# Kernel optimization log

Hardware: AMD Instinct MI355X
Metric: run time of the kernel (lower is better)

Reference implementation:

```python
import jax, jax.numpy as jnp
import numpy as np

B, N, E = 16, 2048, 1024
G, V = 2, 320
D = E // G
TAU = 2.0


def setup_inputs() -> dict:
    key = jax.random.key(0)
    k1, k2, k3, k4 = jax.random.split(key, 4)
    x = jax.random.normal(k1, (B, N, E), dtype=jnp.float32)
    u = jax.random.uniform(k2, (B, N, G, V), dtype=jnp.float32)
    W = jax.random.normal(k3, (E, G * V), dtype=jnp.float32) * 0.02
    b = jnp.zeros((G * V,), dtype=jnp.float32)
    codebook = jax.random.normal(k4, (G, V, D), dtype=jnp.float32)
    return {"x": x, "u": u, "W": W, "b": b, "codebook": codebook}


def reference(x, u, W, b, codebook):
    Bx, Nx, Ex = x.shape
    Gx, Vx, Dx = codebook.shape
    # linear projection -> per-group logits [B,N,G,V]
    h = (jnp.einsum('bne,ef->bnf', x, W) + b).reshape(Bx, Nx, Gx, Vx)
    # gumbel noise from uniform samples (clamped away from 0/1)
    eps = 1e-7
    g = -jnp.log(-jnp.log(u * (1.0 - 2.0 * eps) + eps))
    soft = jax.nn.softmax((h + g) / TAU, axis=-1)
    # hard one-hot with straight-through estimator (matches torch hard=True)
    idx = jnp.argmax(soft, axis=-1)
    hard = jax.nn.one_hot(idx, Vx, dtype=soft.dtype)
    y = hard - jax.lax.stop_gradient(soft) + soft  # [B,N,G,V]
    # select code vectors: equivalent to broadcast-mul + sum over V
    code_vector = jnp.einsum('bngv,gvd->bngd', y, codebook).reshape(Bx, Nx, Gx * Dx)
    # codebook usage entropy: sum one-hots over time, softmax over V per group
    p = jax.nn.softmax(jnp.sum(y, axis=1), axis=-1)  # [B,G,V]
    entropy = -jnp.sum(p * jnp.log(p + 1e-8)) / (Gx * Vx)
    return code_vector, entropy
```

## Files before the change

### kernel.cpp

```cpp
#include <hip/hip_runtime.h>

namespace {

constexpr int Bsz = 16, Nsz = 2048, Esz = 1024, Gsz = 2, Vsz = 320, Dsz = 512;
constexpr int Msz = Bsz * Nsz;
constexpr int Fsz = Gsz * Vsz;
constexpr int BM = 128, BN = 128, BK = 32;
constexpr int NKC = Esz / 32;

typedef __attribute__((ext_vector_type(8))) short bf16x8;
typedef __attribute__((ext_vector_type(4))) float f32x4;
typedef unsigned int u32;
typedef unsigned short u16;

__device__ __forceinline__ void load_lds16(const void* g, void* l) {
  __builtin_amdgcn_global_load_lds(
      (const __attribute__((address_space(1))) u32*)g,
      (__attribute__((address_space(3))) u32*)l, 16, 0, 0);
}

__device__ __forceinline__ ushort f2bf(float f) {
  union { float f; unsigned u; } v; v.f = f;
  unsigned r = (v.u + 0x7FFFu + ((v.u >> 16) & 1u)) >> 16;
  return (ushort)r;
}
__device__ __forceinline__ float bf2f(ushort h) {
  union { unsigned u; float f; } v; v.u = ((unsigned)h) << 16;
  return v.f;
}

__device__ __forceinline__ float gumb_precise(float uu) {
  const float C0 = 1.0f - 2.0f * 1e-7f;
  float up = uu * C0;
  up = up + 1e-7f;
  return -logf(-logf(up));
}
__device__ __forceinline__ float gumb_fast(float uu) {
  const float C0 = 1.0f - 2.0f * 1e-7f;
  const float up = fmaf(uu, C0, 1e-7f);
  const float d = 1.0f - up;
  const float ypoly =
      d * fmaf(d, fmaf(d, fmaf(d, fmaf(d, 0.2f, 0.25f), 0.33333334f), 0.5f), 1.0f);
  const float yfast = -__logf(up);
  const float y = (up >= 0.84f) ? ypoly : yfast;
  return -__logf(y);
}

struct Top2 { float v1, v2; int i1, i2; };
__device__ __forceinline__ void t2_feed(Top2& t, float z, int f) {
  if (z > t.v1 || (z == t.v1 && f < t.i1)) {
    t.v2 = t.v1; t.i2 = t.i1; t.v1 = z; t.i1 = f;
  } else if (z > t.v2 || (z == t.v2 && f < t.i2)) {
    t.v2 = z; t.i2 = f;
  }
}
__device__ __forceinline__ void t2_merge(Top2& t, float ov1, int oi1, float ov2,
                                         int oi2) {
  if (ov1 > t.v1 || (ov1 == t.v1 && oi1 < t.i1)) {
    const bool keep = (t.v1 > ov2) || (t.v1 == ov2 && t.i1 < oi2);
    t.v2 = keep ? t.v1 : ov2; t.i2 = keep ? t.i1 : oi2;
    t.v1 = ov1; t.i1 = oi1;
  } else if (ov1 > t.v2 || (ov1 == t.v2 && oi1 < t.i2)) {
    t.v2 = ov1; t.i2 = oi1;
  }
}

__device__ __forceinline__ uint2 pack_hi_trunc(float4 a) {
  uint2 r;
  r.x = (__float_as_uint(a.x) >> 16) | (__float_as_uint(a.y) & 0xffff0000u);
  r.y = (__float_as_uint(a.z) >> 16) | (__float_as_uint(a.w) & 0xffff0000u);
  return r;
}
__device__ __forceinline__ float4 resid_trunc(float4 a) {
  float4 r;
  r.x = a.x - __uint_as_float(__float_as_uint(a.x) & 0xffff0000u);
  r.y = a.y - __uint_as_float(__float_as_uint(a.y) & 0xffff0000u);
  r.z = a.z - __uint_as_float(__float_as_uint(a.z) & 0xffff0000u);
  r.w = a.w - __uint_as_float(__float_as_uint(a.w) & 0xffff0000u);
  return r;
}


__global__ __launch_bounds__(256) void k_prep(const float* __restrict__ W,
                                              u16* __restrict__ wt,
                                              float* __restrict__ wtT) {
  const int tid = threadIdx.x;
  const int l = tid & 63;
  const int blob = blockIdx.x * 4 + (tid >> 6);
  const int fb = blob >> 5, kc = blob & 31;
  const int f = fb * 16 + (l & 15);
  const int k0 = kc * 32 + (l >> 4) * 8;
  float v[8];
  ushort hh[8], ll[8];
#pragma unroll
  for (int j = 0; j < 8; ++j) {
    v[j] = W[(size_t)(k0 + j) * Fsz + f];
    hh[j] = f2bf(v[j]);
    ll[j] = f2bf(v[j] - bf2f(hh[j]));
  }
  uint4 qh, ql;
  qh.x = hh[0] | ((u32)hh[1] << 16); qh.y = hh[2] | ((u32)hh[3] << 16);
  qh.z = hh[4] | ((u32)hh[5] << 16); qh.w = hh[6] | ((u32)hh[7] << 16);
  ql.x = ll[0] | ((u32)ll[1] << 16); ql.y = ll[2] | ((u32)ll[3] << 16);
  ql.z = ll[4] | ((u32)ll[5] << 16); ql.w = ll[6] | ((u32)ll[7] << 16);
  *(uint4*)(wt + ((size_t)blob * 2 + 0) * 512 + l * 8) = qh;
  *(uint4*)(wt + ((size_t)blob * 2 + 1) * 512 + l * 8) = ql;
  float4 t0, t1;
  t0.x = v[0]; t0.y = v[1]; t0.z = v[2]; t0.w = v[3];
  t1.x = v[4]; t1.y = v[5]; t1.z = v[6]; t1.w = v[7];
  *(float4*)(wtT + (size_t)f * Esz + k0) = t0;
  *(float4*)(wtT + (size_t)f * Esz + k0 + 4) = t1;
}

__global__ __launch_bounds__(256) void k_prepx(const float* __restrict__ x,
                                               u16* __restrict__ xt) {
  const int tid = threadIdx.x;
  const int l = tid & 63;
  const int blob = blockIdx.x * 4 + (tid >> 6);
  const int mb = blob >> 5, kc = blob & 31;
  const size_t row = (size_t)mb * 16 + (l & 15);
  const int k0 = kc * 32 + (l >> 4) * 8;
  const float4 a0 = *(const float4*)(x + row * Esz + k0);
  const float4 a1 = *(const float4*)(x + row * Esz + k0 + 4);
  const uint2 h0 = pack_hi_trunc(a0), h1 = pack_hi_trunc(a1);
  const uint2 l0 = pack_hi_trunc(resid_trunc(a0));
  const uint2 l1 = pack_hi_trunc(resid_trunc(a1));
  uint4 qh, ql;
  qh.x = h0.x; qh.y = h0.y; qh.z = h1.x; qh.w = h1.y;
  ql.x = l0.x; ql.y = l0.y; ql.z = l1.x; ql.w = l1.y;
  *(uint4*)(xt + ((size_t)blob * 2 + 0) * 512 + l * 8) = qh;
  *(uint4*)(xt + ((size_t)blob * 2 + 1) * 512 + l * 8) = ql;
}

__global__ __launch_bounds__(256, 3) void k_gemm(
    const float* __restrict__ u, const float* __restrict__ bias,
    const u16* __restrict__ xt, const u16* __restrict__ wt,
    float4* __restrict__ partial) {
  __shared__ __align__(16) u16 sm[24576];

  const int tid = threadIdx.x;
  const int bid = blockIdx.x;
  const int tile = (bid & 7) * 320 + (bid >> 3);
  const int mt = tile / 10, nt = tile - mt * 10;
  const int m0 = mt * BM;
  const int n0 = nt * 64;

  const int lane = tid & 63, w = tid >> 6;
  const int lrow = lane & 15, quad = lane >> 4;

  f32x4 acc[2][4];
#pragma unroll
  for (int i = 0; i < 2; ++i)
#pragma unroll
    for (int j = 0; j < 4; ++j) acc[i][j] = (f32x4){0.f, 0.f, 0.f, 0.f};

  const u16* src0[6];
  int dstoff[6];
#pragma unroll
  for (int i = 0; i < 6; ++i) {
    const int cc = w + 4 * i;
    const int isA = (cc < 16) ? 1 : 0;
    const int c = isA ? cc : (cc - 16);
    const int gb = (isA ? (m0 >> 4) : (n0 >> 4)) + (c >> 1);
    const int p = c & 1;
    src0[i] = (isA ? xt : wt) + ((size_t)gb * NKC * 2 + p) * 512 + lane * 8;
    dstoff[i] = (isA ? 0 : 8192) + c * 512;
  }

  auto stage = [&](int buf, int kc) {
    const size_t go = (size_t)kc * 1024;
#pragma unroll
    for (int i = 0; i < 6; ++i)
      load_lds16(src0[i] + go, sm + buf * 12288 + dstoff[i]);
  };

  stage(0, 0);
  stage(1, 1);
  int cur = 0;

  for (int kc = 0; kc < NKC; ++kc) {
    if (kc < NKC - 1) {
      asm volatile("s_waitcnt vmcnt(6)" ::: "memory");
    } else {
      asm volatile("s_waitcnt vmcnt(0)" ::: "memory");
    }
    __builtin_amdgcn_s_barrier();

    const u16* As = sm + cur * 12288;
    const u16* Bs = As + 8192;
    bf16x8 ah[2], al[2], bh[4], bl[4];
#pragma unroll
    for (int rt = 0; rt < 2; ++rt) {
      const int blk = w * 2 + rt;
      ah[rt] = *(const bf16x8*)(As + (blk * 2 + 0) * 512 + lane * 8);
      al[rt] = *(const bf16x8*)(As + (blk * 2 + 1) * 512 + lane * 8);
    }
#pragma unroll
    for (int ct = 0; ct < 4; ++ct) {
      bh[ct] = *(const bf16x8*)(Bs + (ct * 2 + 0) * 512 + lane * 8);
      bl[ct] = *(const bf16x8*)(Bs + (ct * 2 + 1) * 512 + lane * 8);
    }
    asm volatile("s_waitcnt lgkmcnt(0)" ::: "memory");
    __builtin_amdgcn_sched_barrier(0);
    __builtin_amdgcn_s_barrier();
    if (kc + 2 < NKC) stage(cur, kc + 2);
    __builtin_amdgcn_sched_barrier(0);
#pragma unroll
    for (int ct = 0; ct < 4; ++ct)
#pragma unroll
      for (int rt = 0; rt < 2; ++rt) {
        acc[rt][ct] = __builtin_amdgcn_mfma_f32_16x16x32_bf16(al[rt], bh[ct], acc[rt][ct], 0, 0, 0);
        acc[rt][ct] = __builtin_amdgcn_mfma_f32_16x16x32_bf16(ah[rt], bl[ct], acc[rt][ct], 0, 0, 0);
        acc[rt][ct] = __builtin_amdgcn_mfma_f32_16x16x32_bf16(ah[rt], bh[ct], acc[rt][ct], 0, 0, 0);
      }
    cur ^= 1;
  }

  const int pcol = nt;
#pragma unroll
  for (int rt = 0; rt < 2; ++rt) {
#pragma unroll
    for (int rg = 0; rg < 4; ++rg) {
      const int row = w * 32 + rt * 16 + quad * 4 + rg;
      const size_t m = (size_t)(m0 + row);
      Top2 t; t.v1 = -3.4e38f; t.v2 = -3.4e38f; t.i1 = 1 << 30; t.i2 = 1 << 30;
#pragma unroll
      for (int ct = 0; ct < 4; ++ct) {
        const int f = n0 + ct * 16 + lrow;
        const float z = acc[rt][ct][rg] + bias[f] + gumb_fast(u[m * 640 + f]);
        t2_feed(t, z, f);
      }
#pragma unroll
      for (int off = 1; off < 16; off <<= 1) {
        const float ov1 = __shfl_xor(t.v1, off, 16);
        const int oi1 = __shfl_xor(t.i1, off, 16);
        const float ov2 = __shfl_xor(t.v2, off, 16);
        const int oi2 = __shfl_xor(t.i2, off, 16);
        t2_merge(t, ov1, oi1, ov2, oi2);
      }
      if (lrow == 0) {
        float4 o;
        o.x = t.v1; o.y = __int_as_float(t.i1);
        o.z = t.v2; o.w = __int_as_float(t.i2);
        partial[m * 10 + pcol] = o;
      }
    }
  }
}

__global__ __launch_bounds__(256) void k_select(
    const float4* __restrict__ partial, const float* __restrict__ x,
    const float* __restrict__ wtT, const float* __restrict__ bias,
    const float* __restrict__ u, int2* __restrict__ idx_out,
    int* __restrict__ counts) {
  const int tid = threadIdx.x;
  const size_t m = (size_t)blockIdx.x * 256 + tid;
  int vsel[2];
#pragma unroll
  for (int g = 0; g < 2; ++g) {
    Top2 t; t.v1 = -3.4e38f; t.v2 = -3.4e38f; t.i1 = 1 << 30; t.i2 = 1 << 30;
#pragma unroll
    for (int p = 0; p < 5; ++p) {
      const float4 q = partial[m * 10 + g * 5 + p];
      t2_merge(t, q.x, __float_as_int(q.y), q.z, __float_as_int(q.w));
    }
    int i1 = t.i1;
    if (t.v1 - t.v2 < 1e-3f) {
      const int i2 = t.i2;
      const float* xp = x + m * Esz;
      const float* w1 = wtT + (size_t)i1 * Esz;
      const float* w2 = wtT + (size_t)i2 * Esz;
      float h1 = 0.f, h2 = 0.f;
      for (int k = 0; k < Esz; k += 4) {
        const float4 xv = *(const float4*)(xp + k);
        const float4 a = *(const float4*)(w1 + k);
        const float4 b = *(const float4*)(w2 + k);
        h1 = fmaf(xv.x, a.x, h1); h1 = fmaf(xv.y, a.y, h1);
        h1 = fmaf(xv.z, a.z, h1); h1 = fmaf(xv.w, a.w, h1);
        h2 = fmaf(xv.x, b.x, h2); h2 = fmaf(xv.y, b.y, h2);
        h2 = fmaf(xv.z, b.z, h2); h2 = fmaf(xv.w, b.w, h2);
      }
      const float z1 = h1 + bias[i1] + gumb_precise(u[m * 640 + i1]);
      const float z2 = h2 + bias[i2] + gumb_precise(u[m * 640 + i2]);
      if (z2 > z1 || (z2 == z1 && i2 < i1)) i1 = i2;
    }
    const int v = i1 - g * Vsz;
    vsel[g] = v;
    const int b = (int)(m >> 11);
    atomicAdd(&counts[(b * Gsz + g) * Vsz + v], 1);
  }
  int2 r; r.x = vsel[0]; r.y = vsel[1];
  idx_out[m] = r;
}

__global__ __launch_bounds__(256) void k_gather(const int2* __restrict__ idx,
                                                const float* __restrict__ cb,
                                                float* __restrict__ out) {
  const int tid = threadIdx.x;
  const size_t mbase = (size_t)blockIdx.x * 8;
  const int gq = tid >> 7, dq = tid & 127;
#pragma unroll
  for (int it = 0; it < 8; ++it) {
    const int2 p = idx[mbase + it];
    const int v = gq ? p.y : p.x;
    const float4 cv =
        *(const float4*)(cb + ((size_t)(gq * Vsz + v)) * Dsz + dq * 4);
    *(float4*)(out + (mbase + it) * (size_t)(Gsz * Dsz) + tid * 4) = cv;
  }
}


__global__ __launch_bounds__(256) void k_prep_fb(const float* __restrict__ W,
                                                 u16* __restrict__ wt_h,
                                                 u16* __restrict__ wt_l) {
  const int f = blockIdx.x;
  const int k0 = threadIdx.x * 4;
  float v[4];
#pragma unroll
  for (int i = 0; i < 4; ++i) v[i] = W[(size_t)(k0 + i) * Fsz + f];
  ushort4 hh, ll;
  hh.x = f2bf(v[0]); ll.x = f2bf(v[0] - bf2f(hh.x));
  hh.y = f2bf(v[1]); ll.y = f2bf(v[1] - bf2f(hh.y));
  hh.z = f2bf(v[2]); ll.z = f2bf(v[2] - bf2f(hh.z));
  hh.w = f2bf(v[3]); ll.w = f2bf(v[3] - bf2f(hh.w));
  *(ushort4*)(wt_h + (size_t)f * Esz + k0) = hh;
  *(ushort4*)(wt_l + (size_t)f * Esz + k0) = ll;
}

__global__ __launch_bounds__(256) void k_gemm_fb(
    const float* __restrict__ x, const float* __restrict__ u,
    const float* __restrict__ bias, const u16* __restrict__ wth,
    const u16* __restrict__ wtl, float4* __restrict__ partial) {
  __shared__ __align__(16) u16 sm[16384];
  u16* xs_h = sm;
  u16* xs_l = sm + 4096;
  u16* bs_h = sm + 8192;
  u16* bs_l = sm + 12288;

  const int tid = threadIdx.x;
  const int n0 = blockIdx.x * BN;
  const int m0 = blockIdx.y * BM;
  const int lane = tid & 63, w = tid >> 6;
  const int wr = w >> 1, wc = w & 1;
  const int lrow = lane & 15, quad = lane >> 4;

  f32x4 acc[4][4];
#pragma unroll
  for (int i = 0; i < 4; ++i)
#pragma unroll
    for (int j = 0; j < 4; ++j) acc[i][j] = (f32x4){0.f, 0.f, 0.f, 0.f};

  for (int k0 = 0; k0 < Esz; k0 += BK) {
    float4 av[4];
#pragma unroll
    for (int s = 0; s < 4; ++s) {
      const int id = tid + 256 * s;
      const int row = id >> 3, kq = id & 7;
      av[s] = *(const float4*)(x + (size_t)(m0 + row) * Esz + k0 + kq * 4);
    }
    __syncthreads();
#pragma unroll
    for (int c = 0; c < 4; ++c) {
      const int chunk = w + 4 * c;
      const int plane = chunk >> 3, ch = chunk & 7;
      const u16* src = (plane ? wtl : wth) +
                       (size_t)(n0 + ch * 16 + (lane >> 2)) * Esz + k0 +
                       (lane & 3) * 8;
      u16* dst = (plane ? bs_l : bs_h) + ch * 512;
      load_lds16(src, dst);
    }
#pragma unroll
    for (int s = 0; s < 4; ++s) {
      const int id = tid + 256 * s;
      const int row = id >> 3, kq = id & 7;
      const u32 u0 = __float_as_uint(av[s].x), u1 = __float_as_uint(av[s].y);
      const u32 u2 = __float_as_uint(av[s].z), u3 = __float_as_uint(av[s].w);
      uint2 hh, ll;
      hh.x = (u0 >> 16) | (u1 & 0xffff0000u);
      hh.y = (u2 >> 16) | (u3 & 0xffff0000u);
      const float r0 = av[s].x - __uint_as_float(u0 & 0xffff0000u);
      const float r1 = av[s].y - __uint_as_float(u1 & 0xffff0000u);
      const float r2 = av[s].z - __uint_as_float(u2 & 0xffff0000u);
      const float r3 = av[s].w - __uint_as_float(u3 & 0xffff0000u);
      ll.x = (__float_as_uint(r0) >> 16) | (__float_as_uint(r1) & 0xffff0000u);
      ll.y = (__float_as_uint(r2) >> 16) | (__float_as_uint(r3) & 0xffff0000u);
      *(uint2*)(xs_h + row * 32 + kq * 4) = hh;
      *(uint2*)(xs_l + row * 32 + kq * 4) = ll;
    }
    __syncthreads();

    bf16x8 ah[4], al[4];
#pragma unroll
    for (int rt = 0; rt < 4; ++rt) {
      const int off = (wr * 64 + rt * 16 + lrow) * 32 + quad * 8;
      ah[rt] = *(const bf16x8*)(xs_h + off);
      al[rt] = *(const bf16x8*)(xs_l + off);
    }
#pragma unroll
    for (int ct = 0; ct < 4; ++ct) {
      const int off = (wc * 64 + ct * 16 + lrow) * 32 + quad * 8;
      const bf16x8 bh = *(const bf16x8*)(bs_h + off);
      const bf16x8 bl = *(const bf16x8*)(bs_l + off);
#pragma unroll
      for (int rt = 0; rt < 4; ++rt) {
        acc[rt][ct] = __builtin_amdgcn_mfma_f32_16x16x32_bf16(al[rt], bh, acc[rt][ct], 0, 0, 0);
        acc[rt][ct] = __builtin_amdgcn_mfma_f32_16x16x32_bf16(ah[rt], bl, acc[rt][ct], 0, 0, 0);
        acc[rt][ct] = __builtin_amdgcn_mfma_f32_16x16x32_bf16(ah[rt], bh, acc[rt][ct], 0, 0, 0);
      }
    }
  }

  const int pcol = blockIdx.x * 2 + wc;
#pragma unroll
  for (int rt = 0; rt < 4; ++rt) {
#pragma unroll
    for (int rg = 0; rg < 4; ++rg) {
      const int row = wr * 64 + rt * 16 + quad * 4 + rg;
      const size_t m = (size_t)(m0 + row);
      Top2 t; t.v1 = -3.4e38f; t.v2 = -3.4e38f; t.i1 = 1 << 30; t.i2 = 1 << 30;
#pragma unroll
      for (int ct = 0; ct < 4; ++ct) {
        const int f = n0 + wc * 64 + ct * 16 + lrow;
        const float z = acc[rt][ct][rg] + bias[f] + gumb_fast(u[m * 640 + f]);
        t2_feed(t, z, f);
      }
#pragma unroll
      for (int off = 1; off < 16; off <<= 1) {
        const float ov1 = __shfl_xor(t.v1, off, 16);
        const int oi1 = __shfl_xor(t.i1, off, 16);
        const float ov2 = __shfl_xor(t.v2, off, 16);
        const int oi2 = __shfl_xor(t.i2, off, 16);
        t2_merge(t, ov1, oi1, ov2, oi2);
      }
      if (lrow == 0) {
        float4 o;
        o.x = t.v1; o.y = __int_as_float(t.i1);
        o.z = t.v2; o.w = __int_as_float(t.i2);
        partial[m * 10 + pcol] = o;
      }
    }
  }
}

__global__ __launch_bounds__(256) void k_select_fb(
    const float4* __restrict__ partial, const float* __restrict__ x,
    const float* __restrict__ W, const float* __restrict__ bias,
    const float* __restrict__ u, const float* __restrict__ cb,
    float* __restrict__ out, int* __restrict__ counts) {
  __shared__ int idx_sh[256][2];
  const int tid = threadIdx.x;
  const size_t m = (size_t)blockIdx.x * 256 + tid;

#pragma unroll
  for (int g = 0; g < 2; ++g) {
    Top2 t; t.v1 = -3.4e38f; t.v2 = -3.4e38f; t.i1 = 1 << 30; t.i2 = 1 << 30;
#pragma unroll
    for (int p = 0; p < 5; ++p) {
      const float4 q = partial[m * 10 + g * 5 + p];
      t2_merge(t, q.x, __float_as_int(q.y), q.z, __float_as_int(q.w));
    }
    int i1 = t.i1;
    if (t.v1 - t.v2 < 1e-3f) {
      const int i2 = t.i2;
      const float* xp = x + m * Esz;
      float h1 = 0.f, h2 = 0.f;
      for (int k = 0; k < Esz; ++k) {
        const float xv = xp[k];
        h1 = fmaf(xv, W[(size_t)k * Fsz + i1], h1);
        h2 = fmaf(xv, W[(size_t)k * Fsz + i2], h2);
      }
      const float z1 = h1 + bias[i1] + gumb_precise(u[m * 640 + i1]);
      const float z2 = h2 + bias[i2] + gumb_precise(u[m * 640 + i2]);
      if (z2 > z1 || (z2 == z1 && i2 < i1)) i1 = i2;
    }
    const int v = i1 - g * Vsz;
    idx_sh[tid][g] = v;
    const int b = (int)(m >> 11);
    atomicAdd(&counts[(b * Gsz + g) * Vsz + v], 1);
  }
  __syncthreads();

  const size_t mbase = (size_t)blockIdx.x * 256;
  const int gq = tid >> 7, dq = tid & 127;
  for (int it = 0; it < 256; ++it) {
    const int v = idx_sh[it][gq];
    const float4 cv =
        *(const float4*)(cb + ((size_t)(gq * Vsz + v)) * Dsz + dq * 4);
    *(float4*)(out + (mbase + it) * (size_t)(Gsz * Dsz) + tid * 4) = cv;
  }
}

__global__ __launch_bounds__(64) void k_entropy(const int* __restrict__ counts,
                                                float* __restrict__ partial) {
  const int bg = blockIdx.x;
  const int lane = threadIdx.x;
  float c[5];
  float mx = -3.4e38f;
#pragma unroll
  for (int t = 0; t < 5; ++t) {
    c[t] = (float)counts[bg * Vsz + lane + 64 * t];
    mx = fmaxf(mx, c[t]);
  }
#pragma unroll
  for (int off = 32; off; off >>= 1) mx = fmaxf(mx, __shfl_xor(mx, off));
  float e[5];
  float s = 0.f;
#pragma unroll
  for (int t = 0; t < 5; ++t) {
    e[t] = expf(c[t] - mx);
    s += e[t];
  }
#pragma unroll
  for (int off = 32; off; off >>= 1) s += __shfl_xor(s, off);
  float ent = 0.f;
#pragma unroll
  for (int t = 0; t < 5; ++t) {
    const float p = e[t] / s;
    ent += p * logf(p + 1e-8f);
  }
#pragma unroll
  for (int off = 32; off; off >>= 1) ent += __shfl_xor(ent, off);
  if (lane == 0) partial[bg] = ent;
}

__global__ __launch_bounds__(64) void k_final(const float* __restrict__ partial,
                                              float* __restrict__ dst) {
  const int lane = threadIdx.x;
  float v = (lane < 32) ? partial[lane] : 0.f;
#pragma unroll
  for (int off = 32; off; off >>= 1) v += __shfl_xor(v, off);
  if (lane == 0) dst[0] = -v / (float)(Gsz * Vsz);
}

}

extern "C" void kernel_launch(void* const* d_in, const int* in_sizes, int n_in,
                              void* d_out, int out_size, void* d_ws,
                              size_t ws_size, hipStream_t stream) {
  const float* x = (const float*)d_in[0];
  const float* u = (const float*)d_in[1];
  const float* W = (const float*)d_in[2];
  const float* bias = (const float*)d_in[3];
  const float* cb = (const float*)d_in[4];
  float* out = (float*)d_out;

  int* counts = (int*)d_ws;
  float* epart = (float*)((char*)d_ws + 40960);
  float4* partial = (float4*)((char*)d_ws + 65536);
  const size_t PART_END = 65536 + (size_t)Msz * 10 * 16;
  const size_t NEED_NEW =
      PART_END + 262144 + 2621440 + 2621440 + (size_t)Msz * Esz * 4;

  hipMemsetAsync(d_ws, 0, 40960, stream);

  if (ws_size >= NEED_NEW) {
    int2* idx = (int2*)((char*)d_ws + PART_END);
    u16* wt = (u16*)((char*)d_ws + PART_END + 262144);
    float* wtT = (float*)((char*)d_ws + PART_END + 262144 + 2621440);
    u16* xt = (u16*)((char*)d_ws + PART_END + 262144 + 2621440 + 2621440);
    k_prep<<<320, 256, 0, stream>>>(W, wt, wtT);
    k_prepx<<<16384, 256, 0, stream>>>(x, xt);
    k_gemm<<<(Msz / BM) * 10, 256, 0, stream>>>(u, bias, xt, wt, partial);
    k_select<<<Msz / 256, 256, 0, stream>>>(partial, x, wtT, bias, u, idx,
                                            counts);
    k_gather<<<Msz / 8, 256, 0, stream>>>(idx, cb, out);
  } else {
    u16* wth = (u16*)((char*)d_ws + PART_END);
    u16* wtl = wth + (size_t)Fsz * Esz;
    k_prep_fb<<<Fsz, 256, 0, stream>>>(W, wth, wtl);
    k_gemm_fb<<<dim3(Fsz / BN, Msz / BM), 256, 0, stream>>>(x, u, bias, wth,
                                                            wtl, partial);
    k_select_fb<<<Msz / 256, 256, 0, stream>>>(partial, x, W, bias, u, cb, out,
                                               counts);
  }
  k_entropy<<<Bsz * Gsz, 64, 0, stream>>>(counts, epart);
  k_final<<<1, 64, 0, stream>>>(epart, out + (size_t)Msz * Esz);
}
```

Before: 540.0 us.

## Load W fragments directly to registers and single-buffer A tile in LDS

Changes the packed x and W layouts to k-major blob order so each k-step is contiguous across row blocks. The GEMM now stages only the A tile through a single LDS buffer and loads B fragments straight from global memory into registers. This cuts LDS use from 48KB to 16KB and raises the launch bound occupancy to 4 blocks per CU, and it adds setprio around the MFMA block. In exchange the pipeline depth drops from double buffering to single buffering with two __syncthreads per step. Each wave also issues its own global loads for B, which exposes more latency.

```diff
diff --git a/kernel.cpp b/kernel.cpp
--- a/kernel.cpp
+++ b/kernel.cpp
@@ -7,6 +7,8 @@
 constexpr int Fsz = Gsz * Vsz;
 constexpr int BM = 128, BN = 128, BK = 32;
 constexpr int NKC = Esz / 32;
+constexpr int NMB = Msz / 16;
+constexpr int NFB = Fsz / 16;
 
 typedef __attribute__((ext_vector_type(8))) short bf16x8;
 typedef __attribute__((ext_vector_type(4))) float f32x4;
@@ -103,8 +105,9 @@
   qh.z = hh[4] | ((u32)hh[5] << 16); qh.w = hh[6] | ((u32)hh[7] << 16);
   ql.x = ll[0] | ((u32)ll[1] << 16); ql.y = ll[2] | ((u32)ll[3] << 16);
   ql.z = ll[4] | ((u32)ll[5] << 16); ql.w = ll[6] | ((u32)ll[7] << 16);
-  *(uint4*)(wt + ((size_t)blob * 2 + 0) * 512 + l * 8) = qh;
-  *(uint4*)(wt + ((size_t)blob * 2 + 1) * 512 + l * 8) = ql;
+  const size_t b2 = (size_t)(kc * NFB + fb);
+  *(uint4*)(wt + (b2 * 2 + 0) * 512 + l * 8) = qh;
+  *(uint4*)(wt + (b2 * 2 + 1) * 512 + l * 8) = ql;
   float4 t0, t1;
   t0.x = v[0]; t0.y = v[1]; t0.z = v[2]; t0.w = v[3];
   t1.x = v[4]; t1.y = v[5]; t1.z = v[6]; t1.w = v[7];
@@ -128,15 +131,16 @@
   uint4 qh, ql;
   qh.x = h0.x; qh.y = h0.y; qh.z = h1.x; qh.w = h1.y;
   ql.x = l0.x; ql.y = l0.y; ql.z = l1.x; ql.w = l1.y;
-  *(uint4*)(xt + ((size_t)blob * 2 + 0) * 512 + l * 8) = qh;
-  *(uint4*)(xt + ((size_t)blob * 2 + 1) * 512 + l * 8) = ql;
-}
-
-__global__ __launch_bounds__(256, 3) void k_gemm(
+  const size_t b2 = (size_t)kc * NMB + mb;
+  *(uint4*)(xt + (b2 * 2 + 0) * 512 + l * 8) = qh;
+  *(uint4*)(xt + (b2 * 2 + 1) * 512 + l * 8) = ql;
+}
+
+__global__ __launch_bounds__(256, 4) void k_gemm(
     const float* __restrict__ u, const float* __restrict__ bias,
     const u16* __restrict__ xt, const u16* __restrict__ wt,
     float4* __restrict__ partial) {
-  __shared__ __align__(16) u16 sm[24576];
+  __shared__ __align__(16) u16 sm[8192];
 
   const int tid = threadIdx.x;
   const int bid = blockIdx.x;
@@ -154,57 +158,46 @@
 #pragma unroll
     for (int j = 0; j < 4; ++j) acc[i][j] = (f32x4){0.f, 0.f, 0.f, 0.f};
 
-  const u16* src0[6];
-  int dstoff[6];
-#pragma unroll
-  for (int i = 0; i < 6; ++i) {
-    const int cc = w + 4 * i;
-    const int isA = (cc < 16) ? 1 : 0;
-    const int c = isA ? cc : (cc - 16);
-    const int gb = (isA ? (m0 >> 4) : (n0 >> 4)) + (c >> 1);
-    const int p = c & 1;
-    src0[i] = (isA ? xt : wt) + ((size_t)gb * NKC * 2 + p) * 512 + lane * 8;
-    dstoff[i] = (isA ? 0 : 8192) + c * 512;
-  }
-
-  auto stage = [&](int buf, int kc) {
-    const size_t go = (size_t)kc * 1024;
-#pragma unroll
-    for (int i = 0; i < 6; ++i)
-      load_lds16(src0[i] + go, sm + buf * 12288 + dstoff[i]);
+  const size_t KSTEP_A = (size_t)NMB * 1024;
+  const size_t KSTEP_B = (size_t)NFB * 1024;
+  const u16* abase = xt + (size_t)(m0 >> 4) * 1024 + lane * 8;
+  const u16* wbase = wt + (size_t)(n0 >> 4) * 1024 + lane * 8;
+
+  auto stageA = [&](int kc) {
+    const u16* s = abase + (size_t)kc * KSTEP_A;
+#pragma unroll
+    for (int i = 0; i < 4; ++i) {
+      const int cc = w + 4 * i;
+      load_lds16(s + cc * 512, sm + cc * 512);
+    }
   };
 
-  stage(0, 0);
-  stage(1, 1);
-  int cur = 0;
+  bf16x8 bh[4], bl[4];
+  auto loadB = [&](int kc) {
+    const u16* s = wbase + (size_t)kc * KSTEP_B;
+#pragma unroll
+    for (int ct = 0; ct < 4; ++ct) {
+      bh[ct] = *(const bf16x8*)(s + ct * 1024);
+      bl[ct] = *(const bf16x8*)(s + ct * 1024 + 512);
+    }
+  };
+
+  stageA(0);
+  loadB(0);
 
   for (int kc = 0; kc < NKC; ++kc) {
-    if (kc < NKC - 1) {
-      asm volatile("s_waitcnt vmcnt(6)" ::: "memory");
-    } else {
-      asm volatile("s_waitcnt vmcnt(0)" ::: "memory");
-    }
-    __builtin_amdgcn_s_barrier();
-
-    const u16* As = sm + cur * 12288;
-    const u16* Bs = As + 8192;
-    bf16x8 ah[2], al[2], bh[4], bl[4];
+    __syncthreads();
+    bf16x8 ah[2], al[2];
 #pragma unroll
     for (int rt = 0; rt < 2; ++rt) {
       const int blk = w * 2 + rt;
-      ah[rt] = *(const bf16x8*)(As + (blk * 2 + 0) * 512 + lane * 8);
-      al[rt] = *(const bf16x8*)(As + (blk * 2 + 1) * 512 + lane * 8);
-    }
-#pragma unroll
-    for (int ct = 0; ct < 4; ++ct) {
-      bh[ct] = *(const bf16x8*)(Bs + (ct * 2 + 0) * 512 + lane * 8);
-      bl[ct] = *(const bf16x8*)(Bs + (ct * 2 + 1) * 512 + lane * 8);
-    }
-    asm volatile("s_waitcnt lgkmcnt(0)" ::: "memory");
+      ah[rt] = *(const bf16x8*)(sm + (blk * 2 + 0) * 512 + lane * 8);
+      al[rt] = *(const bf16x8*)(sm + (blk * 2 + 1) * 512 + lane * 8);
+    }
+    __syncthreads();
+    if (kc + 1 < NKC) stageA(kc + 1);
     __builtin_amdgcn_sched_barrier(0);
-    __builtin_amdgcn_s_barrier();
-    if (kc + 2 < NKC) stage(cur, kc + 2);
-    __builtin_amdgcn_sched_barrier(0);
+    __builtin_amdgcn_s_setprio(1);
 #pragma unroll
     for (int ct = 0; ct < 4; ++ct)
 #pragma unroll
@@ -213,7 +206,8 @@
         acc[rt][ct] = __builtin_amdgcn_mfma_f32_16x16x32_bf16(ah[rt], bl[ct], acc[rt][ct], 0, 0, 0);
         acc[rt][ct] = __builtin_amdgcn_mfma_f32_16x16x32_bf16(ah[rt], bh[ct], acc[rt][ct], 0, 0, 0);
       }
-    cur ^= 1;
+    __builtin_amdgcn_s_setprio(0);
+    if (kc + 1 < NKC) loadB(kc + 1);
   }
 
   const int pcol = nt;
```

New measurement: 549.8 us. About the same (+1.8%).
